# Kernel tuning notes

Hardware: AMD Instinct MI355X
Metric: run time of the kernel (lower is better)

The kernel has to match this reference:

```python
import jax, jax.numpy as jnp
import numpy as np

DN = ('NCHW', 'OIHW', 'NCHW')
SCALES = (4, 2, 5, 2, 1914)  # per-feature one-hot widths; sum=1927, +1 scalar row = 1928 CNN channels


def conv(x, w, b, stride):
    y = jax.lax.conv_general_dilated(x, w, stride, 'VALID', dimension_numbers=DN)
    return y + b[None, :, None, None]


def maxpool(x, window):
    return jax.lax.reduce_window(x, -jnp.inf, jax.lax.max, (1, 1) + window, (1, 1) + window, 'VALID')


def setup_inputs() -> dict:
    key = jax.random.key(0)
    ks = jax.random.split(key, 16)
    B, T, F, H, W = 2, 32, 8, 128, 128
    replay = jax.random.randint(ks[0], (B, T, F, H, W), 0, 2).astype(jnp.float32)

    def rn(k, shape, scale=0.02):
        return jax.random.normal(k, shape, jnp.float32) * scale

    return dict(
        replay_tensor=replay,
        emb_table=rn(ks[1], (16384, 200), 1.0),
        conv_con_w=rn(ks[2], (1, 1, 4, 4)), conv_con_b=jnp.zeros((1,), jnp.float32),
        fc_con_w=rn(ks[3], (200, 961)), fc_con_b=jnp.zeros((200,), jnp.float32),
        cnn1_w=rn(ks[4], (964, 1928, 1, 2)), cnn1_b=jnp.zeros((964,), jnp.float32),
        cnn2_w=rn(ks[5], (482, 964, 1, 2)), cnn2_b=jnp.zeros((482,), jnp.float32),
        cnn3_w=rn(ks[6], (241, 482, 1, 2)), cnn3_b=jnp.zeros((241,), jnp.float32),
        cnn4_w=rn(ks[7], (100, 241, 1, 2)), cnn4_b=jnp.zeros((100,), jnp.float32),
        fc_cnn_w=rn(ks[8], (100, 2300)), fc_cnn_b=jnp.zeros((100,), jnp.float32),
        lstm_w_ih=rn(ks[9], (400, 100), 0.1), lstm_w_hh=rn(ks[10], (400, 100), 0.1),
        lstm_b_ih=jnp.zeros((400,), jnp.float32), lstm_b_hh=jnp.zeros((400,), jnp.float32),
        fc_out_w=rn(ks[11], (2, 100), 0.1), fc_out_b=jnp.zeros((2,), jnp.float32),
        batch_size=2,
    )


def reference(replay_tensor, emb_table, conv_con_w, conv_con_b, fc_con_w, fc_con_b,
              cnn1_w, cnn1_b, cnn2_w, cnn2_b, cnn3_w, cnn3_b, cnn4_w, cnn4_b,
              fc_cnn_w, fc_cnn_b, lstm_w_ih, lstm_w_hh, lstm_b_ih, lstm_b_hh,
              fc_out_w, fc_out_b, batch_size):
    # np.delete(replay, 2, 2) then np.delete(., 3, 2) removes original features 2 and 4
    replay = replay_tensor[:batch_size, :, jnp.array([0, 1, 3, 5, 6, 7])]
    B, T = replay.shape[0], replay.shape[1]
    scalar = replay[:, :, 0]   # [B,T,128,128]
    cat = replay[:, :, 1:6]    # [B,T,5,128,128]

    # --- categorical branch ---
    # The original builds a [scale_k, H*W] one-hot scatter per (b,t,k), then the
    # embedding step reads only spatial column 0: row s of the per-feature block is
    # emb_table[1] iff value_at_pos0 == s (nonzero after thresholding), else emb_table[0].
    v0 = cat[:, :, :, 0, 0].astype(jnp.int32)  # [B,T,5]
    embs = []
    for k, sc in enumerate(SCALES):
        v = v0[:, :, k]
        v = jnp.where(v > sc, 0, v)  # threshold: values > scale_ zeroed
        idx = ((jnp.arange(sc)[None, None, :] == v[:, :, None]) & (v[:, :, None] != 0)).astype(jnp.int32)
        embs.append(emb_table[idx])  # [B,T,sc,200]
    emb_full = jnp.concatenate(embs, axis=2)  # [B,T,1927,200]

    # --- scalar conv branch (faithful to the bug: cnn_con2 applied to raw x) ---
    x = scalar.reshape(B * T, 1, 128, 128)
    y = maxpool(jax.nn.relu(conv(x, conv_con_w, conv_con_b, (2, 2))), (2, 2))  # [BT,1,31,31]
    y = y.reshape(B * T, -1) @ fc_con_w.T + fc_con_b                           # [BT,200]
    sca_full = y.reshape(B, T, 1, 200)

    # --- CNN over concatenated [1928, 1, 200] frames ---
    z = jnp.concatenate([sca_full, emb_full], axis=2).reshape(B * T, 1928, 1, 200)
    z = maxpool(jax.nn.relu(conv(z, cnn1_w, cnn1_b, (1, 1))), (1, 2))
    z = maxpool(jax.nn.relu(conv(z, cnn2_w, cnn2_b, (1, 1))), (1, 2))
    z = maxpool(jax.nn.relu(conv(z, cnn3_w, cnn3_b, (1, 1))), (1, 2))
    z = jax.nn.relu(conv(z, cnn4_w, cnn4_b, (1, 1)))  # [BT,100,1,23]
    z = z.reshape(B * T, -1) @ fc_cnn_w.T + fc_cnn_b  # [BT,100]
    seq = z.reshape(B, T, 100)

    # --- single-layer LSTM (torch gate order i,f,g,o), zero init state ---
    def step(carry, x_t):
        h, c = carry
        g = x_t @ lstm_w_ih.T + h @ lstm_w_hh.T + lstm_b_ih + lstm_b_hh
        i, f, gg, o = jnp.split(g, 4, axis=-1)
        c = jax.nn.sigmoid(f) * c + jax.nn.sigmoid(i) * jnp.tanh(gg)
        h = jax.nn.sigmoid(o) * jnp.tanh(c)
        return (h, c), None

    h0 = jnp.zeros((B, 100), seq.dtype)
    c0 = jnp.zeros((B, 100), seq.dtype)
    (hT, _), _ = jax.lax.scan(step, (h0, c0), jnp.swapaxes(seq, 0, 1))
    return hT @ fc_out_w.T + fc_out_b  # [B,2]
```

## Files before the change

### kernel.cpp

```cpp
#include <hip/hip_runtime.h>
#include <math.h>

#define DEVFN __device__ __forceinline__

typedef __bf16 bf16x8 __attribute__((ext_vector_type(8)));
typedef float f32x4 __attribute__((ext_vector_type(4)));

constexpr int T_ = 32;
constexpr int HW = 128;
constexpr int C1IN = 1928;
constexpr int C1 = 964;

DEVFN float sigm(float x) { return 1.0f / (1.0f + __expf(-x)); }
DEVFN float tanhfast(float x) { return 2.0f / (1.0f + __expf(-2.0f * x)) - 1.0f; }

DEVFN ushort f2b(float v) {
    union { float f; unsigned u; } x; x.f = v;
    unsigned r = x.u + 0x7fffu + ((x.u >> 16) & 1u);
    return (ushort)(r >> 16);
}

DEVFN void gload16(const ushort* g, ushort* l) {
    __builtin_amdgcn_global_load_lds(
        (const __attribute__((address_space(1))) unsigned int*)g,
        (__attribute__((address_space(3))) unsigned int*)l, 16, 0, 0);
}

__global__ void k_front(const float* __restrict__ replay, const float* __restrict__ wc,
                        const float* __restrict__ bc, const float* __restrict__ w1,
                        const float* __restrict__ w2, const float* __restrict__ w3,
                        const float* __restrict__ w4, const float* __restrict__ whh,
                        float* __restrict__ yb, float* __restrict__ wsum,
                        float* __restrict__ sa, ushort* __restrict__ A2,
                        ushort* __restrict__ A3, ushort* __restrict__ A4,
                        float* __restrict__ whhT) {
    const int bid = blockIdx.x;
    const int tx = threadIdx.x;
    constexpr int N2 = 2 * 512 * 1024;
    constexpr int N3 = 2 * 256 * 512;
    constexpr int N4 = 2 * 128 * 256;
    if (bid < 256) {
        const int n = bid >> 2;
        const int idx = (bid & 3) * 256 + tx;
        if (idx >= 961) return;
        const float* x = replay + (size_t)n * 8 * HW * HW;
        float wr_[16];
        #pragma unroll
        for (int t = 0; t < 16; ++t) wr_[t] = wc[t];
        const float bcv = bc[0];
        const int i = idx / 31, j = idx % 31;
        float m = 0.0f;
        #pragma unroll
        for (int di = 0; di < 2; ++di)
        #pragma unroll
        for (int dj = 0; dj < 2; ++dj) {
            const int h0 = 2 * (2 * i + di), w0 = 2 * (2 * j + dj);
            float acc = bcv;
            #pragma unroll
            for (int p = 0; p < 4; ++p)
            #pragma unroll
            for (int q = 0; q < 4; ++q)
                acc += x[(h0 + p) * HW + (w0 + q)] * wr_[p * 4 + q];
            m = fmaxf(m, fmaxf(acc, 0.0f));
        }
        yb[n * 961 + idx] = m;
    } else if (bid < 256 + 5533) {
        const int idx = (bid - 256) * 256 + tx;
        if (idx < N2) {
            const int kw = idx >> 19;
            const int r = idx & 524287;
            const int oc = r >> 10, ic = r & 1023;
            const float v = (oc < 482 && ic < 964) ? w2[(size_t)oc * 1928 + ic * 2 + kw] : 0.f;
            A2[idx] = f2b(v);
        } else if (idx < N2 + N3) {
            const int j = idx - N2;
            const int kw = j >> 17;
            const int r = j & 131071;
            const int oc = r >> 9, ic = r & 511;
            const float v = (oc < 241 && ic < 482) ? w3[(size_t)oc * 964 + ic * 2 + kw] : 0.f;
            A3[j] = f2b(v);
        } else if (idx < N2 + N3 + N4) {
            const int j = idx - (N2 + N3);
            const int kw = j >> 15;
            const int r = j & 32767;
            const int oc = r >> 8, ic = r & 255;
            const float v = (oc < 100 && ic < 241) ? w4[(size_t)oc * 482 + ic * 2 + kw] : 0.f;
            A4[j] = f2b(v);
        } else {
            const int j = idx - (N2 + N3 + N4);
            if (j < 40000) {
                const int m = j / 400, p = j - m * 400;
                const int go = (p & 3) * 100 + (p >> 2);
                whhT[m * 400 + p] = whh[go * 100 + m];
            }
        }
    } else if (bid < 256 + 5774) {
        const int oc = (bid - (256 + 5533)) * 4 + (tx >> 6);
        const int lane = tx & 63;
        const float* wr = w1 + (size_t)oc * C1IN * 2;
        float s0 = 0.f, s1 = 0.f;
        for (int ic = lane; ic < C1IN; ic += 64) {
            s0 += wr[ic * 2 + 0];
            s1 += wr[ic * 2 + 1];
        }
        #pragma unroll
        for (int off = 32; off > 0; off >>= 1) {
            s0 += __shfl_down(s0, off);
            s1 += __shfl_down(s1, off);
        }
        if (lane == 0) { wsum[oc * 2] = s0; wsum[oc * 2 + 1] = s1; }
    } else if (bid < 256 + 6030) {
        const int j = bid - (256 + 5774);
        const int n = j >> 2;
        const int oc = (j & 3) * 256 + tx;
        if (oc < C1) {
            const int chs[5]    = {1, 3, 5, 6, 7};
            const int scales[5] = {4, 2, 5, 2, 1914};
            const int offs[5]   = {0, 4, 6, 11, 13};
            float s0 = 0.f, s1 = 0.f;
            #pragma unroll
            for (int k = 0; k < 5; ++k) {
                int v = (int)replay[((size_t)n * 8 + chs[k]) * HW * HW];
                if (v > scales[k]) v = 0;
                if (v >= 1 && v <= scales[k] - 1) {
                    const int ic = 1 + offs[k] + v;
                    s0 += w1[((size_t)oc * C1IN + ic) * 2 + 0];
                    s1 += w1[((size_t)oc * C1IN + ic) * 2 + 1];
                }
            }
            sa[(n * C1 + oc) * 2 + 0] = s0;
            sa[(n * C1 + oc) * 2 + 1] = s1;
        }
    }
}

__global__ void k_sca_fc(const float* __restrict__ y, const float* __restrict__ fcw,
                         const float* __restrict__ fcb, float* __restrict__ sca) {
    const int n = blockIdx.x;
    const int wid = threadIdx.x >> 6, lane = threadIdx.x & 63;
    const int o = blockIdx.y * 4 + wid;
    float acc = 0.f;
    for (int m = lane; m < 961; m += 64)
        acc += y[n * 961 + m] * fcw[(size_t)o * 961 + m];
    #pragma unroll
    for (int off = 32; off > 0; off >>= 1) acc += __shfl_down(acc, off);
    if (lane == 0) sca[n * 200 + o] = acc + fcb[o];
}

template <int OCT>
__global__ void k_cnn1(const float* __restrict__ sca, const float* __restrict__ emb,
                       const float* __restrict__ w1, const float* __restrict__ b1,
                       const float* __restrict__ wsum, const float* __restrict__ sa,
                       ushort* __restrict__ Bt2) {
    const int n = blockIdx.x;
    const int ocBase = blockIdx.y * OCT;
    const int tx = threadIdx.x;
    __shared__ float ev[200], sv[200], dv[200];
    __shared__ float oscal[OCT][7];
    __shared__ float vals[OCT][100];
    for (int i = tx; i < 200; i += blockDim.x) {
        const float e0 = emb[i], e1 = emb[200 + i];
        ev[i] = e0;
        dv[i] = e1 - e0;
        sv[i] = sca[n * 200 + i] - e0;
    }
    for (int i = tx; i < OCT * 7; i += blockDim.x) {
        const int ocl = i / 7, f = i % 7;
        const int oc = ocBase + ocl;
        float v = 0.f;
        if (oc < C1) {
            switch (f) {
                case 0: v = wsum[oc * 2 + 0]; break;
                case 1: v = wsum[oc * 2 + 1]; break;
                case 2: v = b1[oc]; break;
                case 3: v = w1[(size_t)oc * C1IN * 2 + 0]; break;
                case 4: v = w1[(size_t)oc * C1IN * 2 + 1]; break;
                case 5: v = sa[(n * C1 + oc) * 2 + 0]; break;
                case 6: v = sa[(n * C1 + oc) * 2 + 1]; break;
            }
        }
        oscal[ocl][f] = v;
    }
    __syncthreads();
    for (int item = tx; item < OCT * 99; item += blockDim.x) {
        const int ocl = item / 99, u = item % 99;
        const int oc = ocBase + ocl;
        float res = 0.f;
        if (oc < C1) {
            const float ws0 = oscal[ocl][0], ws1 = oscal[ocl][1], bb = oscal[ocl][2];
            const float a0 = oscal[ocl][3], a1 = oscal[ocl][4];
            const float s0 = oscal[ocl][5], s1 = oscal[ocl][6];
            float r = -INFINITY;
            #pragma unroll
            for (int dw = 0; dw < 2; ++dw) {
                const int ww = 2 * u + dw;
                const float o = bb + ws0 * ev[ww] + ws1 * ev[ww + 1]
                                   + a0 * sv[ww] + a1 * sv[ww + 1]
                                   + s0 * dv[ww] + s1 * dv[ww + 1];
                r = fmaxf(r, o);
            }
            res = fmaxf(r, 0.0f);
        }
        vals[ocl][u] = res;
    }
    __syncthreads();
    for (int i = tx; i < OCT * 100; i += blockDim.x) {
        const int u = i >> 4, ocl = i & 15;
        const float v = (u < 99) ? vals[ocl][u] : 0.0f;
        Bt2[(size_t)(n * 100 + u) * 1024 + ocBase + ocl] = f2b(v);
    }
    if (n == 0 && ocBase == 0) {
        for (int i = tx; i < 1024; i += blockDim.x)
            Bt2[(size_t)6400 * 1024 + i] = 0;
    }
}

template <int OCREAL, int WR, int WOUT, int KICP, int MPAD, int OMODE, int OSTR,
          bool POOL, int MT, int NTILES>
__global__ __launch_bounds__(256, 2) void k_gemm_conv(
    const ushort* __restrict__ A, const ushort* __restrict__ Bt,
    const float* __restrict__ bias, void* __restrict__ outv) {
    constexpr int BK = 64;
    constexpr int NT = KICP / BK;
    constexpr int NWG = MT * NTILES;
    constexpr int Qq = NWG / 8, Rr = NWG % 8;

    __shared__ __align__(16) ushort As0[2][4096];
    __shared__ __align__(16) ushort As1[2][4096];
    __shared__ __align__(16) ushort Bs[2][8704];

    const int bid = blockIdx.x;
    const int xcd = bid & 7, rest = bid >> 3;
    const int base = (xcd < Rr) ? xcd * (Qq + 1) : Rr * (Qq + 1) + (xcd - Rr) * Qq;
    const int sid = base + rest;
    const int mBase = (sid % MT) * 64;
    const int nBase = (sid / MT) * 128;

    const int tx = threadIdx.x;
    const int wave = tx >> 6, lane = tx & 63;
    const int lr = lane & 15, lk = lane >> 4;
    const int r8 = lane >> 3;
    const int cx = (lane & 7) ^ r8;
    const ushort* A1p = A + (size_t)MPAD * KICP;

    f32x4 acc[4][2] = {};

    auto STAGE = [&](int buf, int kt) {
        const int k0 = kt * BK + cx * 8;
        #pragma unroll
        for (int it = 0; it < 2; ++it) {
            const int s = wave + it * 4;
            const int row = s * 8 + r8;
            gload16(&A[(size_t)(mBase + row) * KICP + k0], &As0[buf][s * 512]);
            gload16(&A1p[(size_t)(mBase + row) * KICP + k0], &As1[buf][s * 512]);
        }
        #pragma unroll
        for (int it = 0; it < 4; ++it) {
            const int s = wave + it * 4;
            const int row = s * 8 + r8;
            gload16(&Bt[(size_t)(nBase + row) * KICP + k0], &Bs[buf][s * 512]);
        }
        if (wave == 0) {
            const int row = 128 + r8;
            gload16(&Bt[(size_t)(nBase + row) * KICP + k0], &Bs[buf][16 * 512]);
        }
    };

    auto COMPUTE = [&](int cur) {
        #pragma unroll
        for (int ks = 0; ks < 2; ++ks) {
            bf16x8 a0[4], a1[4], b0[2], b1[2];
            #pragma unroll
            for (int i = 0; i < 4; ++i) {
                const int row = i * 16 + lr;
                const int col = (ks * 32 + lk * 8) ^ ((row & 7) << 3);
                a0[i] = *(const bf16x8*)&As0[cur][row * 64 + col];
                a1[i] = *(const bf16x8*)&As1[cur][row * 64 + col];
            }
            #pragma unroll
            for (int j = 0; j < 2; ++j) {
                const int row = wave * 32 + j * 16 + lr;
                const int col = (ks * 32 + lk * 8) ^ ((row & 7) << 3);
                b0[j] = *(const bf16x8*)&Bs[cur][row * 64 + col];
                const int row1 = row + 1;
                const int col1 = (ks * 32 + lk * 8) ^ ((row1 & 7) << 3);
                b1[j] = *(const bf16x8*)&Bs[cur][row1 * 64 + col1];
            }
            #pragma unroll
            for (int i = 0; i < 4; ++i)
                #pragma unroll
                for (int j = 0; j < 2; ++j) {
                    acc[i][j] = __builtin_amdgcn_mfma_f32_16x16x32_bf16(a0[i], b0[j], acc[i][j], 0, 0, 0);
                    acc[i][j] = __builtin_amdgcn_mfma_f32_16x16x32_bf16(a1[i], b1[j], acc[i][j], 0, 0, 0);
                }
        }
    };

    STAGE(0, 0);
    if (NT > 1) STAGE(1, 1);
    #pragma unroll 1
    for (int kt = 0; kt < NT; ++kt) {
        const int cur = kt & 1;
        if (kt + 1 < NT) {
            if (wave == 0) asm volatile("s_waitcnt vmcnt(9)" ::: "memory");
            else           asm volatile("s_waitcnt vmcnt(8)" ::: "memory");
        } else {
            asm volatile("s_waitcnt vmcnt(0)" ::: "memory");
        }
        __builtin_amdgcn_sched_barrier(0);
        __builtin_amdgcn_s_barrier();
        COMPUTE(cur);
        __builtin_amdgcn_s_barrier();
        if (kt + 2 < NT) STAGE(cur, kt + 2);
    }

    ushort* outb = (ushort*)outv;
    float*  outf = (float*)outv;
    constexpr int NOUTW = POOL ? (WOUT / 2) : WOUT;
    constexpr int WRN = NOUTW + 1;
    constexpr int NVALID = WR * 64;
    #pragma unroll
    for (int i = 0; i < 4; ++i) {
        const int m0 = mBase + i * 16 + lk * 4;
        #pragma unroll
        for (int j = 0; j < 2; ++j) {
            const int r = nBase + wave * 32 + j * 16 + lr;
            const int n = r / WR, w = r - n * WR;
            #pragma unroll
            for (int reg = 0; reg < 4; ++reg) {
                const float v = acc[i][j][reg];
                const float vo = __shfl_xor(v, 1);
                const int m = m0 + reg;
                const bool lok = POOL ? ((lr & 1) == 0) : true;
                if (lok && (w < WOUT) && (m < OCREAL) && (r < NVALID)) {
                    const float pre = POOL ? fmaxf(v, vo) : v;
                    const float val = fmaxf(pre + bias[m], 0.0f);
                    const int wc = POOL ? (w >> 1) : w;
                    if (OMODE == 2)
                        outb[((size_t)(n * WRN + wc)) * OSTR + m] = f2b(val);
                    else
                        outf[((size_t)n * OCREAL + m) * NOUTW + wc] = val;
                }
            }
        }
    }
}

__global__ void k_fc_cnn(const float* __restrict__ z4, const float* __restrict__ w,
                         const float* __restrict__ b, float* __restrict__ seq) {
    const int n = blockIdx.x;
    const int wid = threadIdx.x >> 6, lane = threadIdx.x & 63;
    const int o = blockIdx.y * 4 + wid;
    const float4* zr = (const float4*)(z4 + (size_t)n * 2300);
    const float4* wr = (const float4*)(w + (size_t)o * 2300);
    float acc = 0.f;
    for (int m = lane; m < 575; m += 64) {
        const float4 wv = wr[m];
        const float4 zv = zr[m];
        acc += wv.x * zv.x + wv.y * zv.y + wv.z * zv.z + wv.w * zv.w;
    }
    #pragma unroll
    for (int off = 32; off > 0; off >>= 1) acc += __shfl_down(acc, off);
    if (lane == 0) seq[n * 100 + o] = acc + b[o];
}

__global__ void k_xg(const float* __restrict__ seq, const float* __restrict__ wih,
                     const float* __restrict__ bih, const float* __restrict__ bhh,
                     float* __restrict__ xg) {
    const int n = blockIdx.x;
    __shared__ __align__(16) float s[100];
    if (threadIdx.x < 100) s[threadIdx.x] = seq[n * 100 + threadIdx.x];
    __syncthreads();
    const int p = threadIdx.x;
    if (p < 400) {
        const int go = (p & 3) * 100 + (p >> 2);
        const float4* wr = (const float4*)(wih + (size_t)go * 100);
        const float4* s4 = (const float4*)s;
        float4 a = {0.f, 0.f, 0.f, 0.f};
        #pragma unroll
        for (int m = 0; m < 25; ++m) {
            const float4 wv = wr[m];
            const float4 sv = s4[m];
            a.x += wv.x * sv.x; a.y += wv.y * sv.y;
            a.z += wv.z * sv.z; a.w += wv.w * sv.w;
        }
        xg[n * 400 + p] = bih[go] + bhh[go] + a.x + a.y + a.z + a.w;
    }
}

__global__ __launch_bounds__(448) void k_lstm(const float* __restrict__ xg,
                                              const float* __restrict__ whhT,
                                              const float* __restrict__ fw,
                                              const float* __restrict__ fb,
                                              float* __restrict__ outp) {
    const int bb = blockIdx.x;
    const int tx = threadIdx.x;
    __shared__ __align__(16) float hb[2][104];
    float wreg[100];
    if (tx < 400) {
        #pragma unroll
        for (int m = 0; m < 100; ++m) wreg[m] = whhT[m * 400 + tx];
    }
    float creg = 0.f;
    if (tx < 104) { hb[0][tx] = 0.f; hb[1][tx] = 0.f; }
    float xnext = (tx < 400) ? xg[(size_t)(bb * T_) * 400 + tx] : 0.f;
    __syncthreads();
    const int lane = tx & 63, base = lane & ~3;
    const int g = tx & 3;
    for (int t = 0; t < T_; ++t) {
        float act = 0.f;
        if (tx < 400) {
            float a0 = xnext, a1 = 0.f, a2 = 0.f, a3 = 0.f;
            if (t + 1 < T_) xnext = xg[(size_t)(bb * T_ + t + 1) * 400 + tx];
            const float4* h4 = (const float4*)&hb[t & 1][0];
            #pragma unroll
            for (int m4 = 0; m4 < 25; ++m4) {
                const float4 hv = h4[m4];
                a0 += hv.x * wreg[4 * m4 + 0];
                a1 += hv.y * wreg[4 * m4 + 1];
                a2 += hv.z * wreg[4 * m4 + 2];
                a3 += hv.w * wreg[4 * m4 + 3];
            }
            const float accv = (a0 + a1) + (a2 + a3);
            act = (g == 2) ? tanhfast(accv) : sigm(accv);
        }
        const float aI = __shfl(act, base + 0);
        const float aF = __shfl(act, base + 1);
        const float aG = __shfl(act, base + 2);
        const float aO = __shfl(act, base + 3);
        if (tx < 400) {
            const float cn = aF * creg + aI * aG;
            creg = cn;
            if (g == 0) hb[(t + 1) & 1][tx >> 2] = aO * tanhfast(cn);
        }
        __syncthreads();
    }
    if (tx < 2) {
        float acc = fb[tx];
        for (int j = 0; j < 100; ++j) acc += hb[0][j] * fw[tx * 100 + j];
        outp[bb * 2 + tx] = acc;
    }
}

extern "C" void kernel_launch(void* const* d_in, const int* in_sizes, int n_in,
                              void* d_out, int out_size, void* d_ws, size_t ws_size,
                              hipStream_t stream) {
    (void)in_sizes; (void)n_in; (void)out_size; (void)ws_size;
    const float* replay = (const float*)d_in[0];
    const float* emb    = (const float*)d_in[1];
    const float* ccw    = (const float*)d_in[2];
    const float* ccb    = (const float*)d_in[3];
    const float* fcw    = (const float*)d_in[4];
    const float* fcb    = (const float*)d_in[5];
    const float* w1     = (const float*)d_in[6];
    const float* b1     = (const float*)d_in[7];
    const float* w2     = (const float*)d_in[8];
    const float* b2     = (const float*)d_in[9];
    const float* w3     = (const float*)d_in[10];
    const float* b3     = (const float*)d_in[11];
    const float* w4     = (const float*)d_in[12];
    const float* b4     = (const float*)d_in[13];
    const float* fcnw   = (const float*)d_in[14];
    const float* fcnb   = (const float*)d_in[15];
    const float* wih    = (const float*)d_in[16];
    const float* whh    = (const float*)d_in[17];
    const float* bih    = (const float*)d_in[18];
    const float* bhh    = (const float*)d_in[19];
    const float* fow    = (const float*)d_in[20];
    const float* fob    = (const float*)d_in[21];

    float* ws = (float*)d_ws;
    float*  sca  = ws + 0;
    float*  wsum = ws + 12800;
    float*  sa   = ws + 14848;
    float*  seq  = ws + 138240;
    float*  xg   = ws + 144640;
    float*  whhT = ws + 170240;
    float*  yb   = ws + 210240;
    float*  z4   = ws + 272384;
    ushort* A2   = (ushort*)(ws + 419584);
    ushort* A3   = (ushort*)(ws + 943872);
    ushort* A4   = (ushort*)(ws + 1074944);
    ushort* Bt2  = (ushort*)(ws + 1107712);
    ushort* Bt3  = (ushort*)(ws + 4385024);
    ushort* Bt4  = (ushort*)(ws + 5208320);
    float*  outp = (float*)d_out;

    k_front<<<6286, 256, 0, stream>>>(replay, ccw, ccb, w1, w2, w3, w4, whh,
                                      yb, wsum, sa, A2, A3, A4, whhT);
    k_sca_fc<<<dim3(64, 50), 256, 0, stream>>>(yb, fcw, fcb, sca);
    k_cnn1<16><<<dim3(64, 64), 256, 0, stream>>>(sca, emb, w1, b1, wsum, sa, Bt2);
    k_gemm_conv<482, 100, 98, 1024, 512, 2, 512, true, 8, 50>
        <<<400, 256, 0, stream>>>(A2, Bt2, b2, Bt3);
    k_gemm_conv<241, 50, 48, 512, 256, 2, 256, true, 4, 25>
        <<<100, 256, 0, stream>>>(A3, Bt3, b3, Bt4);
    k_gemm_conv<100, 25, 23, 256, 128, 0, 0, false, 2, 13>
        <<<26, 256, 0, stream>>>(A4, Bt4, b4, z4);
    k_fc_cnn<<<dim3(64, 25), 256, 0, stream>>>(z4, fcnw, fcnb, seq);
    k_xg<<<64, 512, 0, stream>>>(seq, wih, bih, bhh, xg);
    k_lstm<<<2, 448, 0, stream>>>(xg, whhT, fow, fob, outp);
}
```

Baseline: 136.9 us.

## Fuse small-conv+FC into front kernel and fc_cnn with LSTM input gates

The small conv/pool stage and its 961->200 FC now run together in front-kernel blocks. Each block recomputes the pooled conv map into shared memory and then produces 4 FC outputs, so the separate k_sca_fc launch goes away. Likewise, the fc_cnn projection and the LSTM input-gate GEMM are merged into one kernel that keeps seq in shared memory, removing two launches and the intermediate global buffers. The cost is redundant conv work: each batch item's conv is recomputed 50 times. The fused FC kernel also has far fewer blocks, so each thread does longer serial dot products.

After: 185.7 us. 1.36x slower.

```diff
diff --git a/kernel.cpp b/kernel.cpp
--- a/kernel.cpp
+++ b/kernel.cpp
@@ -27,10 +27,11 @@
 }
 
 __global__ void k_front(const float* __restrict__ replay, const float* __restrict__ wc,
-                        const float* __restrict__ bc, const float* __restrict__ w1,
+                        const float* __restrict__ bc, const float* __restrict__ fcw,
+                        const float* __restrict__ fcb, const float* __restrict__ w1,
                         const float* __restrict__ w2, const float* __restrict__ w3,
                         const float* __restrict__ w4, const float* __restrict__ whh,
-                        float* __restrict__ yb, float* __restrict__ wsum,
+                        float* __restrict__ sca, float* __restrict__ wsum,
                         float* __restrict__ sa, ushort* __restrict__ A2,
                         ushort* __restrict__ A3, ushort* __restrict__ A4,
                         float* __restrict__ whhT) {
@@ -39,33 +40,9 @@
     constexpr int N2 = 2 * 512 * 1024;
     constexpr int N3 = 2 * 256 * 512;
     constexpr int N4 = 2 * 128 * 256;
-    if (bid < 256) {
-        const int n = bid >> 2;
-        const int idx = (bid & 3) * 256 + tx;
-        if (idx >= 961) return;
-        const float* x = replay + (size_t)n * 8 * HW * HW;
-        float wr_[16];
-        #pragma unroll
-        for (int t = 0; t < 16; ++t) wr_[t] = wc[t];
-        const float bcv = bc[0];
-        const int i = idx / 31, j = idx % 31;
-        float m = 0.0f;
-        #pragma unroll
-        for (int di = 0; di < 2; ++di)
-        #pragma unroll
-        for (int dj = 0; dj < 2; ++dj) {
-            const int h0 = 2 * (2 * i + di), w0 = 2 * (2 * j + dj);
-            float acc = bcv;
-            #pragma unroll
-            for (int p = 0; p < 4; ++p)
-            #pragma unroll
-            for (int q = 0; q < 4; ++q)
-                acc += x[(h0 + p) * HW + (w0 + q)] * wr_[p * 4 + q];
-            m = fmaxf(m, fmaxf(acc, 0.0f));
-        }
-        yb[n * 961 + idx] = m;
-    } else if (bid < 256 + 5533) {
-        const int idx = (bid - 256) * 256 + tx;
+    __shared__ __align__(16) float ys[961];
+    if (bid < 5533) {
+        const int idx = bid * 256 + tx;
         if (idx < N2) {
             const int kw = idx >> 19;
             const int r = idx & 524287;
@@ -94,8 +71,8 @@
                 whhT[m * 400 + p] = whh[go * 100 + m];
             }
         }
-    } else if (bid < 256 + 5774) {
-        const int oc = (bid - (256 + 5533)) * 4 + (tx >> 6);
+    } else if (bid < 5774) {
+        const int oc = (bid - 5533) * 4 + (tx >> 6);
         const int lane = tx & 63;
         const float* wr = w1 + (size_t)oc * C1IN * 2;
         float s0 = 0.f, s1 = 0.f;
@@ -109,8 +86,8 @@
             s1 += __shfl_down(s1, off);
         }
         if (lane == 0) { wsum[oc * 2] = s0; wsum[oc * 2 + 1] = s1; }
-    } else if (bid < 256 + 6030) {
-        const int j = bid - (256 + 5774);
+    } else if (bid < 6030) {
+        const int j = bid - 5774;
         const int n = j >> 2;
         const int oc = (j & 3) * 256 + tx;
         if (oc < C1) {
@@ -131,20 +108,43 @@
             sa[(n * C1 + oc) * 2 + 0] = s0;
             sa[(n * C1 + oc) * 2 + 1] = s1;
         }
-    }
-}
-
-__global__ void k_sca_fc(const float* __restrict__ y, const float* __restrict__ fcw,
-                         const float* __restrict__ fcb, float* __restrict__ sca) {
-    const int n = blockIdx.x;
-    const int wid = threadIdx.x >> 6, lane = threadIdx.x & 63;
-    const int o = blockIdx.y * 4 + wid;
-    float acc = 0.f;
-    for (int m = lane; m < 961; m += 64)
-        acc += y[n * 961 + m] * fcw[(size_t)o * 961 + m];
-    #pragma unroll
-    for (int off = 32; off > 0; off >>= 1) acc += __shfl_down(acc, off);
-    if (lane == 0) sca[n * 200 + o] = acc + fcb[o];
+    } else {
+        const int sid = bid - 6030;
+        const int n = sid / 50;
+        const int o0 = (sid - n * 50) * 4;
+        const float* x = replay + (size_t)n * 8 * HW * HW;
+        float wr_[16];
+        #pragma unroll
+        for (int t = 0; t < 16; ++t) wr_[t] = wc[t];
+        const float bcv = bc[0];
+        for (int idx = tx; idx < 961; idx += 256) {
+            const int i = idx / 31, j = idx % 31;
+            float m = 0.0f;
+            #pragma unroll
+            for (int di = 0; di < 2; ++di)
+            #pragma unroll
+            for (int dj = 0; dj < 2; ++dj) {
+                const int h0 = 2 * (2 * i + di), w0 = 2 * (2 * j + dj);
+                float acc = bcv;
+                #pragma unroll
+                for (int p = 0; p < 4; ++p)
+                #pragma unroll
+                for (int q = 0; q < 4; ++q)
+                    acc += x[(h0 + p) * HW + (w0 + q)] * wr_[p * 4 + q];
+                m = fmaxf(m, fmaxf(acc, 0.0f));
+            }
+            ys[idx] = m;
+        }
+        __syncthreads();
+        const int wid = tx >> 6, lane = tx & 63;
+        const int o = o0 + wid;
+        float acc = 0.f;
+        for (int m = lane; m < 961; m += 64)
+            acc += ys[m] * fcw[(size_t)o * 961 + m];
+        #pragma unroll
+        for (int off = 32; off > 0; off >>= 1) acc += __shfl_down(acc, off);
+        if (lane == 0) sca[n * 200 + o] = acc + fcb[o];
+    }
 }
 
 template <int OCT>
@@ -346,36 +346,34 @@
     }
 }
 
-__global__ void k_fc_cnn(const float* __restrict__ z4, const float* __restrict__ w,
-                         const float* __restrict__ b, float* __restrict__ seq) {
+__global__ __launch_bounds__(512) void k_seq_xg(
+    const float* __restrict__ z4, const float* __restrict__ fcnw,
+    const float* __restrict__ fcnb, const float* __restrict__ wih,
+    const float* __restrict__ bih, const float* __restrict__ bhh,
+    float* __restrict__ xg) {
     const int n = blockIdx.x;
-    const int wid = threadIdx.x >> 6, lane = threadIdx.x & 63;
-    const int o = blockIdx.y * 4 + wid;
-    const float4* zr = (const float4*)(z4 + (size_t)n * 2300);
-    const float4* wr = (const float4*)(w + (size_t)o * 2300);
-    float acc = 0.f;
-    for (int m = lane; m < 575; m += 64) {
-        const float4 wv = wr[m];
-        const float4 zv = zr[m];
-        acc += wv.x * zv.x + wv.y * zv.y + wv.z * zv.z + wv.w * zv.w;
-    }
-    #pragma unroll
-    for (int off = 32; off > 0; off >>= 1) acc += __shfl_down(acc, off);
-    if (lane == 0) seq[n * 100 + o] = acc + b[o];
-}
-
-__global__ void k_xg(const float* __restrict__ seq, const float* __restrict__ wih,
-                     const float* __restrict__ bih, const float* __restrict__ bhh,
-                     float* __restrict__ xg) {
-    const int n = blockIdx.x;
-    __shared__ __align__(16) float s[100];
-    if (threadIdx.x < 100) s[threadIdx.x] = seq[n * 100 + threadIdx.x];
+    const int tx = threadIdx.x;
+    __shared__ __align__(16) float seqs[100];
+    if (tx < 400) {
+        const int o = tx >> 2, l = tx & 3;
+        const float4* zr = (const float4*)(z4 + (size_t)n * 2300);
+        const float4* wr = (const float4*)(fcnw + (size_t)o * 2300);
+        float acc = 0.f;
+        for (int m = l; m < 575; m += 4) {
+            const float4 wv = wr[m];
+            const float4 zv = zr[m];
+            acc += wv.x * zv.x + wv.y * zv.y + wv.z * zv.z + wv.w * zv.w;
+        }
+        acc += __shfl_xor(acc, 1);
+        acc += __shfl_xor(acc, 2);
+        if (l == 0) seqs[o] = acc + fcnb[o];
+    }
     __syncthreads();
-    const int p = threadIdx.x;
-    if (p < 400) {
+    if (tx < 400) {
+        const int p = tx;
         const int go = (p & 3) * 100 + (p >> 2);
         const float4* wr = (const float4*)(wih + (size_t)go * 100);
-        const float4* s4 = (const float4*)s;
+        const float4* s4 = (const float4*)seqs;
         float4 a = {0.f, 0.f, 0.f, 0.f};
         #pragma unroll
         for (int m = 0; m < 25; ++m) {
@@ -473,22 +471,20 @@
     float*  sca  = ws + 0;
     float*  wsum = ws + 12800;
     float*  sa   = ws + 14848;
-    float*  seq  = ws + 138240;
-    float*  xg   = ws + 144640;
-    float*  whhT = ws + 170240;
-    float*  yb   = ws + 210240;
-    float*  z4   = ws + 272384;
-    ushort* A2   = (ushort*)(ws + 419584);
-    ushort* A3   = (ushort*)(ws + 943872);
-    ushort* A4   = (ushort*)(ws + 1074944);
-    ushort* Bt2  = (ushort*)(ws + 1107712);
-    ushort* Bt3  = (ushort*)(ws + 4385024);
-    ushort* Bt4  = (ushort*)(ws + 5208320);
+    float*  xg   = ws + 138240;
+    float*  whhT = ws + 163840;
+    float*  z4   = ws + 203840;
+    ushort* A2   = (ushort*)(ws + 351040);
+    ushort* A3   = (ushort*)(ws + 875328);
+    ushort* A4   = (ushort*)(ws + 1006400);
+    ushort* Bt2  = (ushort*)(ws + 1039168);
+    ushort* Bt3  = (ushort*)(ws + 4316480);
+    ushort* Bt4  = (ushort*)(ws + 5139776);
     float*  outp = (float*)d_out;
 
-    k_front<<<6286, 256, 0, stream>>>(replay, ccw, ccb, w1, w2, w3, w4, whh,
-                                      yb, wsum, sa, A2, A3, A4, whhT);
-    k_sca_fc<<<dim3(64, 50), 256, 0, stream>>>(yb, fcw, fcb, sca);
+    k_front<<<9230, 256, 0, stream>>>(replay, ccw, ccb, fcw, fcb,
+                                      w1, w2, w3, w4, whh,
+                                      sca, wsum, sa, A2, A3, A4, whhT);
     k_cnn1<16><<<dim3(64, 64), 256, 0, stream>>>(sca, emb, w1, b1, wsum, sa, Bt2);
     k_gemm_conv<482, 100, 98, 1024, 512, 2, 512, true, 8, 50>
         <<<400, 256, 0, stream>>>(A2, Bt2, b2, Bt3);
@@ -496,7 +492,6 @@
         <<<100, 256, 0, stream>>>(A3, Bt3, b3, Bt4);
     k_gemm_conv<100, 25, 23, 256, 128, 0, 0, false, 2, 13>
         <<<26, 256, 0, stream>>>(A4, Bt4, b4, z4);
-    k_fc_cnn<<<dim3(64, 25), 256, 0, stream>>>(z4, fcnw, fcnb, seq);
-    k_xg<<<64, 512, 0, stream>>>(seq, wih, bih, bhh, xg);
+    k_seq_xg<<<64, 512, 0, stream>>>(z4, fcnw, fcnb, wih, bih, bhh, xg);
     k_lstm<<<2, 448, 0, stream>>>(xg, whhT, fow, fob, outp);
 }
```
